# Optimization experiments

Measured on AMD Instinct MI355X. Metric: run time of the kernel, lower is better.

Reference implementation:

```python
import jax, jax.numpy as jnp
import numpy as np

N_P = 32  # top-N_p points kept per channel
EPS = 1e-5  # BatchNorm eps


def setup_inputs() -> dict:
    key = jax.random.key(0)
    ks = jax.random.split(key, 20)
    B, N = 16, 8192
    d = {"x": jax.random.normal(ks[0], (B, 3, N), dtype=jnp.float32)}
    dims = [(64, 3), (128, 64), (256, 128)]
    i = 1
    for li, (co, ci) in enumerate(dims, start=1):
        d[f"w{li}"] = jax.random.normal(ks[i], (co, ci), dtype=jnp.float32) * (1.0 / np.sqrt(ci)); i += 1
        d[f"b{li}"] = jax.random.normal(ks[i], (co,), dtype=jnp.float32) * 0.1; i += 1
        d[f"g{li}"] = jax.random.uniform(ks[i], (co,), dtype=jnp.float32, minval=0.5, maxval=1.5); i += 1
        d[f"be{li}"] = jax.random.normal(ks[i], (co,), dtype=jnp.float32) * 0.1; i += 1
        d[f"m{li}"] = jax.random.normal(ks[i], (co,), dtype=jnp.float32) * 0.1; i += 1
        d[f"v{li}"] = jax.random.uniform(ks[i], (co,), dtype=jnp.float32, minval=0.5, maxval=1.5); i += 1
    return d


def _conv_bn(h, w, b, g, be, m, v, relu):
    # Conv1d with kernel_size=1 == per-point linear: [B,Ci,N] x [Co,Ci] -> [B,Co,N]
    h = jnp.einsum('bin,oi->bon', h, w) + b[None, :, None]
    h = (h - m[None, :, None]) * (g[None, :, None] / jnp.sqrt(v[None, :, None] + EPS)) + be[None, :, None]
    return jax.nn.relu(h) if relu else h


def reference(x, w1, b1, g1, be1, m1, v1, w2, b2, g2, be2, m2, v2, w3, b3, g3, be3, m3, v3):
    h = _conv_bn(x, w1, b1, g1, be1, m1, v1, True)
    h = _conv_bn(h, w2, b2, g2, be2, m2, v2, True)
    h = _conv_bn(h, w3, b3, g3, be3, m3, v3, False)  # [B,C,N], C=256
    # SoftPool: per-channel top-N_p point indices, gather all channels at them
    _, idx = jax.lax.top_k(h, N_P)  # idx: [B,C,N_p] (descending sort == top_k)
    # gathered[b, c_sort, c_feat, k] = h[b, c_feat, idx[b, c_sort, k]]
    gathered = jnp.take_along_axis(h[:, None, :, :], idx[:, :, None, :], axis=3)  # [B,C,C,N_p]
    # sp_cube[b, c_feat, k, c_sort]
    return gathered.transpose(0, 2, 3, 1)
```

## Files before the change

kernel.cpp:

```cpp
#include <hip/hip_runtime.h>


using v4f = __attribute__((ext_vector_type(4))) float;

__device__ __forceinline__ float bf16rne(float x) {
    unsigned u = __float_as_uint(x);
    u = (u + 0x7FFFu + ((u >> 16) & 1u)) & 0xFFFF0000u;
    return __uint_as_float(u);
}

__global__ void scales_kernel(const float* __restrict__ g1, const float* __restrict__ v1,
                              const float* __restrict__ g2, const float* __restrict__ v2,
                              const float* __restrict__ g3, const float* __restrict__ v3,
                              float* __restrict__ s) {
    int t = threadIdx.x;
    if (t < 64)       s[t] = __fdiv_rn(g1[t],       __fsqrt_rn(__fadd_rn(v1[t],       1e-5f)));
    else if (t < 192) s[t] = __fdiv_rn(g2[t - 64],  __fsqrt_rn(__fadd_rn(v2[t - 64],  1e-5f)));
    else if (t < 448) s[t] = __fdiv_rn(g3[t - 192], __fsqrt_rn(__fadd_rn(v3[t - 192], 1e-5f)));
}

__global__ void w3t_kernel(const float* __restrict__ w3, float* __restrict__ w3t) {
    int i = blockIdx.x * 256 + threadIdx.x;
    int o = i >> 7, k = i & 127;
    int q = k >> 2, c = k & 3;
    int tile = o >> 4, j = o & 15;
    w3t[(((q * 16 + tile) * 16 + j) << 2) + c] = w3[o * 128 + k];
}

__global__ __launch_bounds__(256, 1) void mlp12_kernel(
        const float* __restrict__ x,
        const float* __restrict__ w1, const float* __restrict__ b1,
        const float* __restrict__ m1, const float* __restrict__ be1,
        const float* __restrict__ w2, const float* __restrict__ b2,
        const float* __restrict__ m2, const float* __restrict__ be2,
        const float* __restrict__ sc,
        float* __restrict__ h2g) {
    const float* s1 = sc;
    const float* s2 = sc + 64;

    int t    = threadIdx.x;
    int tile = blockIdx.x & 3;
    int pt   = (blockIdx.x >> 2) * 256 + t;
    int b    = pt >> 13;
    int n    = pt & 8191;

    const float* xb = x + (size_t)b * 24576 + n;
    float x0 = xb[0], x1 = xb[8192], x2 = xb[16384];

    float h1[64];
#pragma unroll
    for (int o = 0; o < 64; ++o) {
        float acc = __fmul_rn(w1[o * 3 + 0], x0);
        acc = __fadd_rn(acc, __fmul_rn(w1[o * 3 + 1], x1));
        acc = __fadd_rn(acc, __fmul_rn(w1[o * 3 + 2], x2));
        float hpb = __fadd_rn(acc, b1[o]);
        float tt  = __fsub_rn(hpb, m1[o]);
        float r   = __fadd_rn(__fmul_rn(tt, s1[o]), be1[o]);
        h1[o] = fmaxf(r, 0.0f);
    }

    v4f* dst = (v4f*)h2g;
    const v4f* w2v = (const v4f*)w2;
    for (int qq = 0; qq < 8; ++qq) {
        int q = tile * 8 + qq;
        v4f hv;
#pragma unroll
        for (int j = 0; j < 4; ++j) {
            int c2 = q * 4 + j;
            const v4f* wr = w2v + c2 * 16;
            float a = 0.0f;
#pragma unroll
            for (int k = 0; k < 16; ++k) {
                v4f w = wr[k];
                a = __fadd_rn(a, __fmul_rn(w.x, h1[4 * k + 0]));
                a = __fadd_rn(a, __fmul_rn(w.y, h1[4 * k + 1]));
                a = __fadd_rn(a, __fmul_rn(w.z, h1[4 * k + 2]));
                a = __fadd_rn(a, __fmul_rn(w.w, h1[4 * k + 3]));
            }
            float hpb = __fadd_rn(a, b2[c2]);
            float tt  = __fsub_rn(hpb, m2[c2]);
            hv[j] = fmaxf(__fadd_rn(__fmul_rn(tt, s2[c2]), be2[c2]), 0.0f);
        }
        dst[(size_t)q * 131072 + pt] = hv;
    }
}

__global__ __launch_bounds__(256) void mlp3_kernel(
        const float* __restrict__ h2g,
        const float* __restrict__ w3t, const float* __restrict__ b3,
        const float* __restrict__ m3, const float* __restrict__ be3,
        const float* __restrict__ sc,
        float* __restrict__ h) {
    const float* s3 = sc + 192;

    int B    = blockIdx.x;
    int xcd  = B & 7;
    int slot = B >> 3;
    int tile = slot & 15;
    int ptb  = (slot >> 4) * 8 + xcd;
    int t    = threadIdx.x;
    int pt   = ptb * 256 + t;
    int b    = pt >> 13;
    int n    = pt & 8191;
    int ob   = tile * 16;

    float acc[16];
#pragma unroll
    for (int j = 0; j < 16; ++j) acc[j] = 0.0f;

    const v4f* src  = (const v4f*)h2g;
    const v4f* w3tv = (const v4f*)w3t;

    for (int q = 0; q < 32; ++q) {
        v4f hv = src[(size_t)q * 131072 + pt];
        const v4f* wq = w3tv + (size_t)(q * 16 + tile) * 16;
#pragma unroll
        for (int j = 0; j < 16; ++j) {
            v4f w = wq[j];
            acc[j] = __fadd_rn(acc[j], __fmul_rn(w.x, hv.x));
            acc[j] = __fadd_rn(acc[j], __fmul_rn(w.y, hv.y));
            acc[j] = __fadd_rn(acc[j], __fmul_rn(w.z, hv.z));
            acc[j] = __fadd_rn(acc[j], __fmul_rn(w.w, hv.w));
        }
    }

    float* hb = h + (size_t)b * 2097152 + n;
#pragma unroll
    for (int j = 0; j < 16; ++j) {
        int o = ob + j;
        float hpb = __fadd_rn(acc[j], b3[o]);
        float tt  = __fsub_rn(hpb, m3[o]);
        float rr  = __fadd_rn(__fmul_rn(tt, s3[o]), be3[o]);
        hb[(size_t)o * 8192] = rr;
    }
}

__global__ __launch_bounds__(256) void topk_kernel(const float* __restrict__ h,
                                                   int* __restrict__ idx_out) {
    __shared__ unsigned long long mrg[2][64][4];

    int t      = threadIdx.x;
    int lane   = t & 63;
    int waveid = (t >> 6) & 1;
    int rhalf  = t >> 7;
    int row    = blockIdx.x * 2 + rhalf;
    const float* hr = h + (size_t)row * 8192;
    const v4f* hv4  = (const v4f*)hr;

    unsigned long long k0 = 0, k1 = 0, k2 = 0, k3 = 0;
    int j0 = waveid * 16;
    int lanebase = 8191 - lane * 4;

    v4f p0 = hv4[(j0 + 0) * 64 + lane], p1 = hv4[(j0 + 1) * 64 + lane];
    v4f p2 = hv4[(j0 + 2) * 64 + lane], p3 = hv4[(j0 + 3) * 64 + lane];

    for (int jb = 0; jb < 4; ++jb) {
        int jn = j0 + ((jb < 3) ? (jb + 1) * 4 : 0);
        v4f n0 = hv4[(jn + 0) * 64 + lane], n1 = hv4[(jn + 1) * 64 + lane];
        v4f n2 = hv4[(jn + 2) * 64 + lane], n3 = hv4[(jn + 3) * 64 + lane];

#pragma unroll
        for (int jj = 0; jj < 4; ++jj) {
            v4f v = (jj == 0) ? p0 : (jj == 1) ? p1 : (jj == 2) ? p2 : p3;
            int j = j0 + jb * 4 + jj;
#pragma unroll
            for (int c = 0; c < 4; ++c) {
                unsigned u = __float_as_uint(v[c]);
                u = (u & 0x80000000u) ? ~u : (u | 0x80000000u);
                unsigned long long key =
                    ((unsigned long long)u << 13) |
                    (unsigned)(lanebase - (j * 256 + c));
                unsigned long long s = key, hi;
                hi = (k0 > s) ? k0 : s;  s = (k0 > s) ? s : k0;  k0 = hi;
                hi = (k1 > s) ? k1 : s;  s = (k1 > s) ? s : k1;  k1 = hi;
                hi = (k2 > s) ? k2 : s;  s = (k2 > s) ? s : k2;  k2 = hi;
                k3 = (k3 > s) ? k3 : s;
            }
        }
        p0 = n0; p1 = n1; p2 = n2; p3 = n3;
    }

    if (waveid == 1) {
        mrg[rhalf][lane][0] = k0; mrg[rhalf][lane][1] = k1;
        mrg[rhalf][lane][2] = k2; mrg[rhalf][lane][3] = k3;
    }
    __syncthreads();
    if (waveid == 1) return;

#pragma unroll
    for (int q = 0; q < 4; ++q) {
        unsigned long long s = mrg[rhalf][lane][q], hi;
        hi = (k0 > s) ? k0 : s;  s = (k0 > s) ? s : k0;  k0 = hi;
        hi = (k1 > s) ? k1 : s;  s = (k1 > s) ? s : k1;  k1 = hi;
        hi = (k2 > s) ? k2 : s;  s = (k2 > s) ? s : k2;  k2 = hi;
        k3 = (k3 > s) ? k3 : s;
    }

    unsigned long long last = 0xFFFFFFFFFFFFFFFFull;
    int valid = 4;

    for (int pass = 0; pass < 32; ++pass) {
        unsigned long long m = k0;
#pragma unroll
        for (int s = 1; s < 64; s <<= 1) {
            unsigned long long o = __shfl_xor(m, s, 64);
            m = (o > m) ? o : m;
        }
        if (lane == 0) idx_out[row * 32 + pass] = 8191 - (int)(m & 8191ull);

        if (k0 == m) {
            last = m;
            k0 = k1; k1 = k2; k2 = k3; k3 = 0ull;
            --valid;
            if (valid == 0 && pass < 31) {
                for (int j = 0; j < 32; ++j) {
                    v4f v = *(const v4f*)&hr[j * 256 + lane * 4];
#pragma unroll
                    for (int c = 0; c < 4; ++c) {
                        unsigned u = __float_as_uint(v[c]);
                        u = (u & 0x80000000u) ? ~u : (u | 0x80000000u);
                        int i = j * 256 + lane * 4 + c;
                        unsigned long long key = ((unsigned long long)u << 13) | (unsigned)(8191 - i);
                        if (key < last && key > k3) {
                            unsigned long long s = key, hi;
                            hi = (k0 > s) ? k0 : s;  s = (k0 > s) ? s : k0;  k0 = hi;
                            hi = (k1 > s) ? k1 : s;  s = (k1 > s) ? s : k1;  k1 = hi;
                            hi = (k2 > s) ? k2 : s;  s = (k2 > s) ? s : k2;  k2 = hi;
                            k3 = s;
                        }
                    }
                }
                valid = 4;
            }
        }
    }
}

__global__ __launch_bounds__(256) void gather_kernel(const float* __restrict__ h,
                                                     const int* __restrict__ idx,
                                                     float* __restrict__ out) {
    __shared__ int   idxs2[8192];
    __shared__ float hlds[8192];

    int blk = blockIdx.x;
    int b   = blk >> 6;
    int cfq = blk & 63;
    int t   = threadIdx.x;

    for (int d = t; d < 8192; d += 256) {
        int k = d >> 8, cs = d & 255;
        idxs2[d] = idx[b * 8192 + cs * 32 + k];
    }

    const float* hb = h + (size_t)b * 2097152;
    float* ob = out + (size_t)b * 2097152;

#pragma unroll
    for (int r = 0; r < 4; ++r) {
        int cf = cfq * 4 + r;
        const float* hrow = hb + (size_t)cf * 8192;
        float* orow = ob + (size_t)cf * 8192;

        const v4f* hr4 = (const v4f*)hrow;
#pragma unroll
        for (int s = 0; s < 8; ++s) {
            v4f v = hr4[s * 256 + t];
            *(v4f*)&hlds[(s * 256 + t) * 4] = v;
        }
        __syncthreads();

#pragma unroll 8
        for (int rep = 0; rep < 32; ++rep) {
            int elem = rep * 256 + t;
            int i = idxs2[elem];
            orow[elem] = bf16rne(hlds[i]);
        }
        __syncthreads();
    }
}

extern "C" void kernel_launch(void* const* d_in, const int* in_sizes, int n_in,
                              void* d_out, int out_size, void* d_ws, size_t ws_size,
                              hipStream_t stream) {
    const float* x   = (const float*)d_in[0];
    const float* w1  = (const float*)d_in[1];
    const float* b1  = (const float*)d_in[2];
    const float* g1  = (const float*)d_in[3];
    const float* be1 = (const float*)d_in[4];
    const float* m1  = (const float*)d_in[5];
    const float* v1  = (const float*)d_in[6];
    const float* w2  = (const float*)d_in[7];
    const float* b2  = (const float*)d_in[8];
    const float* g2  = (const float*)d_in[9];
    const float* be2 = (const float*)d_in[10];
    const float* m2  = (const float*)d_in[11];
    const float* v2  = (const float*)d_in[12];
    const float* w3  = (const float*)d_in[13];
    const float* b3  = (const float*)d_in[14];
    const float* g3  = (const float*)d_in[15];
    const float* be3 = (const float*)d_in[16];
    const float* m3  = (const float*)d_in[17];
    const float* v3  = (const float*)d_in[18];

    char* ws = (char*)d_ws;
    float* h    = (float*)(ws);
    int*   idxb = (int*)(ws + 134217728);
    float* sc   = (float*)(ws + 134742016);
    float* w3t  = (float*)(ws + 134744064);
    float* h2g  = (float*)d_out;

    scales_kernel<<<1, 448, 0, stream>>>(g1, v1, g2, v2, g3, v3, sc);
    w3t_kernel<<<128, 256, 0, stream>>>(w3, w3t);
    mlp12_kernel<<<2048, 256, 0, stream>>>(x, w1, b1, m1, be1,
                                           w2, b2, m2, be2, sc, h2g);
    mlp3_kernel<<<8192, 256, 0, stream>>>(h2g, w3t, b3, m3, be3, sc, h);
    topk_kernel<<<2048, 256, 0, stream>>>(h, idxb);
    gather_kernel<<<1024, 256, 0, stream>>>(h, idxb, (float*)d_out);
}
```

Before: 277.3 us.

## Fuse layer-2 and layer-3 MLP kernels via shared-memory staging of h2

Merges mlp12 and mlp3 into one kernel. Each block handles 64 points: four wave-quarters compute layer-2 channels into a 32 KB shared buffer, then each thread computes 64 of the 256 layer-3 outputs from shared memory. This removes the 64 MB global write and re-read of the intermediate h2. The cost is fewer points per block, only 2048 blocks with launch_bounds(256,1), and layer-3 weights reloaded per block, which may lower occupancy and weight-load efficiency.

```diff
diff --git a/kernel.cpp b/kernel.cpp
--- a/kernel.cpp
+++ b/kernel.cpp
@@ -27,22 +27,28 @@
     w3t[(((q * 16 + tile) * 16 + j) << 2) + c] = w3[o * 128 + k];
 }
 
-__global__ __launch_bounds__(256, 1) void mlp12_kernel(
+__global__ __launch_bounds__(256, 1) void mlpf_kernel(
         const float* __restrict__ x,
         const float* __restrict__ w1, const float* __restrict__ b1,
         const float* __restrict__ m1, const float* __restrict__ be1,
         const float* __restrict__ w2, const float* __restrict__ b2,
         const float* __restrict__ m2, const float* __restrict__ be2,
+        const float* __restrict__ w3t, const float* __restrict__ b3,
+        const float* __restrict__ m3, const float* __restrict__ be3,
         const float* __restrict__ sc,
-        float* __restrict__ h2g) {
+        float* __restrict__ h) {
+    __shared__ v4f h2s[2048];
+
     const float* s1 = sc;
     const float* s2 = sc + 64;
-
-    int t    = threadIdx.x;
-    int tile = blockIdx.x & 3;
-    int pt   = (blockIdx.x >> 2) * 256 + t;
-    int b    = pt >> 13;
-    int n    = pt & 8191;
+    const float* s3 = sc + 192;
+
+    int t       = threadIdx.x;
+    int pt_l    = t & 63;
+    int quarter = t >> 6;
+    int pt      = blockIdx.x * 64 + pt_l;
+    int b       = pt >> 13;
+    int n       = pt & 8191;
 
     const float* xb = x + (size_t)b * 24576 + n;
     float x0 = xb[0], x1 = xb[8192], x2 = xb[16384];
@@ -59,10 +65,9 @@
         h1[o] = fmaxf(r, 0.0f);
     }
 
-    v4f* dst = (v4f*)h2g;
     const v4f* w2v = (const v4f*)w2;
     for (int qq = 0; qq < 8; ++qq) {
-        int q = tile * 8 + qq;
+        int q = quarter * 8 + qq;
         v4f hv;
 #pragma unroll
         for (int j = 0; j < 4; ++j) {
@@ -81,57 +86,46 @@
             float tt  = __fsub_rn(hpb, m2[c2]);
             hv[j] = fmaxf(__fadd_rn(__fmul_rn(tt, s2[c2]), be2[c2]), 0.0f);
         }
-        dst[(size_t)q * 131072 + pt] = hv;
-    }
-}
-
-__global__ __launch_bounds__(256) void mlp3_kernel(
-        const float* __restrict__ h2g,
-        const float* __restrict__ w3t, const float* __restrict__ b3,
-        const float* __restrict__ m3, const float* __restrict__ be3,
-        const float* __restrict__ sc,
-        float* __restrict__ h) {
-    const float* s3 = sc + 192;
-
-    int B    = blockIdx.x;
-    int xcd  = B & 7;
-    int slot = B >> 3;
-    int tile = slot & 15;
-    int ptb  = (slot >> 4) * 8 + xcd;
-    int t    = threadIdx.x;
-    int pt   = ptb * 256 + t;
-    int b    = pt >> 13;
-    int n    = pt & 8191;
-    int ob   = tile * 16;
-
-    float acc[16];
-#pragma unroll
-    for (int j = 0; j < 16; ++j) acc[j] = 0.0f;
-
-    const v4f* src  = (const v4f*)h2g;
+        h2s[q * 64 + pt_l] = hv;
+    }
+    __syncthreads();
+
     const v4f* w3tv = (const v4f*)w3t;
-
-    for (int q = 0; q < 32; ++q) {
-        v4f hv = src[(size_t)q * 131072 + pt];
-        const v4f* wq = w3tv + (size_t)(q * 16 + tile) * 16;
-#pragma unroll
-        for (int j = 0; j < 16; ++j) {
-            v4f w = wq[j];
-            acc[j] = __fadd_rn(acc[j], __fmul_rn(w.x, hv.x));
-            acc[j] = __fadd_rn(acc[j], __fmul_rn(w.y, hv.y));
-            acc[j] = __fadd_rn(acc[j], __fmul_rn(w.z, hv.z));
-            acc[j] = __fadd_rn(acc[j], __fmul_rn(w.w, hv.w));
-        }
-    }
-
     float* hb = h + (size_t)b * 2097152 + n;
-#pragma unroll
-    for (int j = 0; j < 16; ++j) {
-        int o = ob + j;
-        float hpb = __fadd_rn(acc[j], b3[o]);
-        float tt  = __fsub_rn(hpb, m3[o]);
-        float rr  = __fadd_rn(__fmul_rn(tt, s3[o]), be3[o]);
-        hb[(size_t)o * 8192] = rr;
+
+    for (int tp = 0; tp < 4; ++tp) {
+        float acc[16];
+#pragma unroll
+        for (int j = 0; j < 16; ++j) acc[j] = 0.0f;
+
+        for (int q = 0; q < 32; ++q) {
+            v4f hv = h2s[q * 64 + pt_l];
+            const v4f* wq = w3tv + (size_t)(q * 16 + tp * 4) * 16 + quarter * 4;
+#pragma unroll
+            for (int c = 0; c < 4; ++c) {
+                const v4f* wt = wq + c * 16;
+#pragma unroll
+                for (int jj = 0; jj < 4; ++jj) {
+                    v4f w = wt[jj];
+                    acc[c * 4 + jj] = __fadd_rn(acc[c * 4 + jj], __fmul_rn(w.x, hv.x));
+                    acc[c * 4 + jj] = __fadd_rn(acc[c * 4 + jj], __fmul_rn(w.y, hv.y));
+                    acc[c * 4 + jj] = __fadd_rn(acc[c * 4 + jj], __fmul_rn(w.z, hv.z));
+                    acc[c * 4 + jj] = __fadd_rn(acc[c * 4 + jj], __fmul_rn(w.w, hv.w));
+                }
+            }
+        }
+
+#pragma unroll
+        for (int c = 0; c < 4; ++c) {
+#pragma unroll
+            for (int jj = 0; jj < 4; ++jj) {
+                int o = (tp * 4 + c) * 16 + quarter * 4 + jj;
+                float hpb = __fadd_rn(acc[c * 4 + jj], b3[o]);
+                float tt  = __fsub_rn(hpb, m3[o]);
+                float rr  = __fadd_rn(__fmul_rn(tt, s3[o]), be3[o]);
+                hb[(size_t)o * 8192] = rr;
+            }
+        }
     }
 }
 
@@ -307,13 +301,12 @@
     int*   idxb = (int*)(ws + 134217728);
     float* sc   = (float*)(ws + 134742016);
     float* w3t  = (float*)(ws + 134744064);
-    float* h2g  = (float*)d_out;
 
     scales_kernel<<<1, 448, 0, stream>>>(g1, v1, g2, v2, g3, v3, sc);
     w3t_kernel<<<128, 256, 0, stream>>>(w3, w3t);
-    mlp12_kernel<<<2048, 256, 0, stream>>>(x, w1, b1, m1, be1,
-                                           w2, b2, m2, be2, sc, h2g);
-    mlp3_kernel<<<8192, 256, 0, stream>>>(h2g, w3t, b3, m3, be3, sc, h);
+    mlpf_kernel<<<2048, 256, 0, stream>>>(x, w1, b1, m1, be1,
+                                          w2, b2, m2, be2,
+                                          w3t, b3, m3, be3, sc, h);
     topk_kernel<<<2048, 256, 0, stream>>>(h, idxb);
     gather_kernel<<<1024, 256, 0, stream>>>(h, idxb, (float*)d_out);
 }
```

Result: slower. 736.5 us (+165.6%).
